# Optimization experiments

Measured on AMD Instinct MI355X. Metric: run time of the kernel, lower is better.

## Reference

```python
import jax, jax.numpy as jnp
import numpy as np

B, N, C, OUT, K2 = 64, 4096, 64, 64, 4  # batch, lattice sites, in/out features, kersize^2

def setup_inputs() -> dict:
    key = jax.random.key(0)
    k1, k2, k3, k4 = jax.random.split(key, 4)
    std = 0.5 / jnp.sqrt(K2 * (C + OUT))  # matches module's init stddev (W_scale=b_scale=1)
    x = jax.random.normal(k1, (B, N, C), dtype=jnp.float32)
    W = jax.random.normal(k2, (K2, C, OUT), dtype=jnp.float32) * std
    b = jax.random.normal(k3, (OUT,), dtype=jnp.float32) * std
    kernel2 = jax.random.randint(k4, (N, K2), 0, N, dtype=jnp.int32)
    return {"x": x, "W": W, "b": b, "kernel2": kernel2}

def reference(x, W, b, kernel2):
    # gather neighbors: [B, N, K2, C]; contract (K2, C) with W -> [B, N, OUT]
    y = jnp.einsum('bnkc,kco->bno', x[:, kernel2, :], W)
    # bias broadcast (original used tensordot with ones([B,N]))
    return y + b
```

## Files before the change

kernel.cpp:

```cpp
#include <hip/hip_runtime.h>
#include <stdint.h>


#define N_SITES  4096
#define C_DIM    64
#define OUT_DIM  64

typedef __attribute__((ext_vector_type(8))) short bf16x8;
typedef __attribute__((ext_vector_type(4))) float f32x4;

__device__ __forceinline__ uint32_t pack2_bf16(float f0, float f1) {
    uint32_t u0 = __float_as_uint(f0) + 0x8000u;
    uint32_t u1 = __float_as_uint(f1) + 0x8000u;
    return __builtin_amdgcn_perm(u1, u0, 0x07060302u);
}

template<int N> __device__ __forceinline__ void wait_vmcnt() {
    asm volatile("s_waitcnt vmcnt(%0)" :: "n"(N) : "memory");
}

template<int OFF>
__device__ __forceinline__ void gld16(f32x4& d, const float* p) {
    asm volatile("global_load_dwordx4 %0, %1, off offset:%2"
                 : "=v"(d) : "v"(p), "n"(OFF) : "memory");
}

__host__ __device__ constexpr int wait_for(int i) {
    return (i == 0 || i == 1) ? 16
         : (i == 2)           ? 20
         : (i == 14)          ? 16
         : (i == 15)          ? 4
         : (i & 1)            ? 20
         : 24;
}

__global__ __launch_bounds__(64, 1)
void conv_vgather_kernel(const float* __restrict__ x, const float* __restrict__ W,
                         const float* __restrict__ bias, const int* __restrict__ kernel2,
                         float* __restrict__ out)
{
    __shared__ __align__(16) int lds_idx[32 * 4];

    const int lane = threadIdx.x;
    const int bi   = blockIdx.x;
    const int half = bi >> 10;
    const int r    = bi & 1023;
    const int bgl  = r & 7;
    const int sg   = r >> 3;
    const int bg   = bgl + half * 8;
    const int n0   = sg * 32;
    const int b0   = bg * 4;

    const int c  = lane & 15;
    const int q  = lane >> 4;
    const int sl = c >> 2;
    const int bb = c & 3;

    if (lane < 32)
        ((int4*)lds_idx)[lane] = ((const int4*)kernel2)[n0 + lane];

    bf16x8 aw[4][8];
    #pragma unroll
    for (int t = 0; t < 4; ++t)
        #pragma unroll
        for (int s = 0; s < 8; ++s) {
            uint32_t* ap = (uint32_t*)&aw[t][s];
            #pragma unroll
            for (int u = 0; u < 4; ++u) {
                float f0 = W[(size_t)(s*32 + q*8 + 2*u    ) * OUT_DIM + t*16 + c];
                float f1 = W[(size_t)(s*32 + q*8 + 2*u + 1) * OUT_DIM + t*16 + c];
                ap[u] = pack2_bf16(f0, f1);
            }
        }

    f32x4 bias_r[4];
    #pragma unroll
    for (int t = 0; t < 4; ++t) bias_r[t] = *(const f32x4*)&bias[t*16 + q*4];

    const float* gxb = x + (size_t)(b0 + bb) * (N_SITES * C_DIM) + q * 8;

    wait_vmcnt<0>();
    __builtin_amdgcn_sched_barrier(0);

    f32x4 buf0[8], buf1[8], buf2[8];

    auto issue = [&](f32x4* buf, int i) {
        const int2 tk = *(const int2*)&lds_idx[(i >> 1) * 16 + sl * 4 + (i & 1) * 2];
        const float* p0 = gxb + (size_t)(uint32_t)tk.x * C_DIM;
        const float* p1 = gxb + (size_t)(uint32_t)tk.y * C_DIM;
        gld16<0>(buf[0], p0); gld16<16>(buf[1], p0);
        gld16<128>(buf[2], p0); gld16<144>(buf[3], p0);
        gld16<0>(buf[4], p1); gld16<16>(buf[5], p1);
        gld16<128>(buf[6], p1); gld16<144>(buf[7], p1);
    };

    auto comp = [&](const f32x4* buf, int h, f32x4* acc) {
        #pragma unroll
        for (int tl = 0; tl < 2; ++tl)
            #pragma unroll
            for (int hs = 0; hs < 2; ++hs) {
                const f32x4 xa = buf[tl*4 + hs*2];
                const f32x4 xb = buf[tl*4 + hs*2 + 1];
                bf16x8 bf;
                uint32_t* bp = (uint32_t*)&bf;
                bp[0] = pack2_bf16(xa[0], xa[1]);
                bp[1] = pack2_bf16(xa[2], xa[3]);
                bp[2] = pack2_bf16(xb[0], xb[1]);
                bp[3] = pack2_bf16(xb[2], xb[3]);
                #pragma unroll
                for (int t = 0; t < 4; ++t)
                    acc[t] = __builtin_amdgcn_mfma_f32_16x16x32_bf16(
                        aw[t][h*4 + tl*2 + hs], bf, acc[t], 0, 0, 0);
            }
    };

    auto dostore = [&](int p, const f32x4* acc) {
        const int n = n0 + p * 4 + sl;
        float* op = out + ((size_t)(b0 + bb) * N_SITES + n) * OUT_DIM + q * 4;
        #pragma unroll
        for (int t = 0; t < 4; ++t)
            *(f32x4*)(op + t*16) = acc[t] + bias_r[t];
    };

    issue(buf0, 0);
    issue(buf1, 1);
    issue(buf2, 2);

    f32x4 acc[4];

    #define STEP(i)                                                           \
    {                                                                         \
        wait_vmcnt<wait_for(i)>();                                            \
        __builtin_amdgcn_sched_barrier(0);                                    \
        f32x4* bcur = ((i) % 3 == 0) ? buf0 : ((i) % 3 == 1) ? buf1 : buf2;   \
        if (((i) & 1) == 0) {                                                 \
            acc[0] = (f32x4){0.f,0.f,0.f,0.f};                                \
            acc[1] = (f32x4){0.f,0.f,0.f,0.f};                                \
            acc[2] = (f32x4){0.f,0.f,0.f,0.f};                                \
            acc[3] = (f32x4){0.f,0.f,0.f,0.f};                                \
        }                                                                     \
        comp(bcur, (i) & 1, acc);                                             \
        if ((i) <= 12) issue(bcur, (i) + 3);                                  \
        if ((i) & 1) dostore((i) >> 1, acc);                                  \
    }

    STEP(0);  STEP(1);  STEP(2);  STEP(3);
    STEP(4);  STEP(5);  STEP(6);  STEP(7);
    STEP(8);  STEP(9);  STEP(10); STEP(11);
    STEP(12); STEP(13); STEP(14); STEP(15);

    #undef STEP
}

extern "C" void kernel_launch(void* const* d_in, const int* in_sizes, int n_in,
                              void* d_out, int out_size, void* d_ws, size_t ws_size,
                              hipStream_t stream) {
    const float* x       = (const float*)d_in[0];
    const float* W       = (const float*)d_in[1];
    const float* bias    = (const float*)d_in[2];
    const int*   kernel2 = (const int*)d_in[3];
    float* out = (float*)d_out;

    conv_vgather_kernel<<<2048, 64, 0, stream>>>(x, W, bias, kernel2, out);
}
```

Measured before the change: 146.0 us.

## Split neighbor gathers between direct-to-LDS loads and register loads

Each pipeline step now sends one of its two gathered neighbor rows through global_load_lds_dwordx4 into a triple-buffered, XOR-swizzled LDS tile. The other row still goes through ordinary global loads into registers. The compute stage reads the LDS half with ds_reads before converting to bf16 for the MFMAs. The aim is to cut VGPR buffer pressure and spread load traffic across two paths. The cost is extra LDS traffic, m0 setup per load, and reliance on vmcnt ordering to know when LDS writes are visible.

```diff
diff --git a/kernel.cpp b/kernel.cpp
--- a/kernel.cpp
+++ b/kernel.cpp
@@ -17,6 +17,12 @@
 
 template<int N> __device__ __forceinline__ void wait_vmcnt() {
     asm volatile("s_waitcnt vmcnt(%0)" :: "n"(N) : "memory");
+}
+
+__device__ __forceinline__ void gll16(const float* p, uint32_t m0v) {
+    asm volatile("s_mov_b32 m0, %1\n\t"
+                 "global_load_lds_dwordx4 %0, off"
+                 :: "v"(p), "s"(m0v) : "memory");
 }
 
 template<int OFF>
@@ -35,11 +41,11 @@
 }
 
 __global__ __launch_bounds__(64, 1)
-void conv_vgather_kernel(const float* __restrict__ x, const float* __restrict__ W,
-                         const float* __restrict__ bias, const int* __restrict__ kernel2,
-                         float* __restrict__ out)
+void conv_dual_kernel(const float* __restrict__ x, const float* __restrict__ W,
+                      const float* __restrict__ bias, const int* __restrict__ kernel2,
+                      float* __restrict__ out)
 {
-    __shared__ __align__(16) int lds_idx[32 * 4];
+    __shared__ __align__(1024) uint8_t lds_raw[12800];
 
     const int lane = threadIdx.x;
     const int bi   = blockIdx.x;
@@ -56,8 +62,12 @@
     const int sl = c >> 2;
     const int bb = c & 3;
 
+    const int g = lane >> 4;
+    const int u = lane & 15;
+
     if (lane < 32)
-        ((int4*)lds_idx)[lane] = ((const int4*)kernel2)[n0 + lane];
+        ((int4*)(lds_raw + 12288))[lane] = ((const int4*)kernel2)[n0 + lane];
+    const int* lds_idx = (const int*)(lds_raw + 12288);
 
     bf16x8 aw[4][8];
     #pragma unroll
@@ -66,10 +76,10 @@
         for (int s = 0; s < 8; ++s) {
             uint32_t* ap = (uint32_t*)&aw[t][s];
             #pragma unroll
-            for (int u = 0; u < 4; ++u) {
-                float f0 = W[(size_t)(s*32 + q*8 + 2*u    ) * OUT_DIM + t*16 + c];
-                float f1 = W[(size_t)(s*32 + q*8 + 2*u + 1) * OUT_DIM + t*16 + c];
-                ap[u] = pack2_bf16(f0, f1);
+            for (int uu = 0; uu < 4; ++uu) {
+                float f0 = W[(size_t)(s*32 + q*8 + 2*uu    ) * OUT_DIM + t*16 + c];
+                float f1 = W[(size_t)(s*32 + q*8 + 2*uu + 1) * OUT_DIM + t*16 + c];
+                ap[uu] = pack2_bf16(f0, f1);
             }
         }
 
@@ -77,41 +87,69 @@
     #pragma unroll
     for (int t = 0; t < 4; ++t) bias_r[t] = *(const f32x4*)&bias[t*16 + q*4];
 
+    const float* gxn = x + (size_t)(b0 + g) * (N_SITES * C_DIM)
+                     + (size_t)((((u >> 1) ^ g) * 8) + (u & 1) * 4);
     const float* gxb = x + (size_t)(b0 + bb) * (N_SITES * C_DIM) + q * 8;
+
+    const uint32_t lds0 =
+        __builtin_amdgcn_readfirstlane((uint32_t)(uintptr_t)lds_raw);
 
     wait_vmcnt<0>();
     __builtin_amdgcn_sched_barrier(0);
 
-    f32x4 buf0[8], buf1[8], buf2[8];
-
-    auto issue = [&](f32x4* buf, int i) {
-        const int2 tk = *(const int2*)&lds_idx[(i >> 1) * 16 + sl * 4 + (i & 1) * 2];
-        const float* p0 = gxb + (size_t)(uint32_t)tk.x * C_DIM;
-        const float* p1 = gxb + (size_t)(uint32_t)tk.y * C_DIM;
-        gld16<0>(buf[0], p0); gld16<16>(buf[1], p0);
-        gld16<128>(buf[2], p0); gld16<144>(buf[3], p0);
-        gld16<0>(buf[4], p1); gld16<16>(buf[5], p1);
-        gld16<128>(buf[6], p1); gld16<144>(buf[7], p1);
+    f32x4 vb0[4], vb1[4], vb2[4];
+
+    auto issue = [&](f32x4* vb, int i) {
+        const int pp = i >> 1, h = i & 1;
+        const int* ib = lds_idx + pp * 16;
+        const uint32_t m0s = lds0 + (uint32_t)(i % 3) * 4096;
+        #pragma unroll
+        for (int slp = 0; slp < 4; ++slp) {
+            const int nka = ib[slp * 4 + 2 * h];
+            const float* rowa = gxn + (size_t)(uint32_t)nka * C_DIM;
+            gll16(rowa, m0s + (uint32_t)slp * 1024);
+        }
+        const int nkb = ib[sl * 4 + 2 * h + 1];
+        const float* rowb = gxb + (size_t)(uint32_t)nkb * C_DIM;
+        gld16<0>(vb[0], rowb);   gld16<16>(vb[1], rowb);
+        gld16<128>(vb[2], rowb); gld16<144>(vb[3], rowb);
     };
 
-    auto comp = [&](const f32x4* buf, int h, f32x4* acc) {
-        #pragma unroll
-        for (int tl = 0; tl < 2; ++tl)
+    auto comp = [&](const f32x4* vb, int i, f32x4* acc) {
+        const uint32_t tb = (uint32_t)(i % 3) * 4096;
+        const int h = i & 1;
+        #pragma unroll
+        for (int hs = 0; hs < 2; ++hs) {
+            const uint8_t* pb = lds_raw + tb + (uint32_t)c * 256
+                              + (uint32_t)(((hs * 4 + q) ^ (c & 3)) * 32);
+            f32x4 xa = *(const f32x4*)(pb);
+            f32x4 xb = *(const f32x4*)(pb + 16);
+            bf16x8 bf;
+            uint32_t* bp = (uint32_t*)&bf;
+            bp[0] = pack2_bf16(xa[0], xa[1]);
+            bp[1] = pack2_bf16(xa[2], xa[3]);
+            bp[2] = pack2_bf16(xb[0], xb[1]);
+            bp[3] = pack2_bf16(xb[2], xb[3]);
             #pragma unroll
-            for (int hs = 0; hs < 2; ++hs) {
-                const f32x4 xa = buf[tl*4 + hs*2];
-                const f32x4 xb = buf[tl*4 + hs*2 + 1];
-                bf16x8 bf;
-                uint32_t* bp = (uint32_t*)&bf;
-                bp[0] = pack2_bf16(xa[0], xa[1]);
-                bp[1] = pack2_bf16(xa[2], xa[3]);
-                bp[2] = pack2_bf16(xb[0], xb[1]);
-                bp[3] = pack2_bf16(xb[2], xb[3]);
-                #pragma unroll
-                for (int t = 0; t < 4; ++t)
-                    acc[t] = __builtin_amdgcn_mfma_f32_16x16x32_bf16(
-                        aw[t][h*4 + tl*2 + hs], bf, acc[t], 0, 0, 0);
-            }
+            for (int t = 0; t < 4; ++t)
+                acc[t] = __builtin_amdgcn_mfma_f32_16x16x32_bf16(
+                    aw[t][h*4 + hs], bf, acc[t], 0, 0, 0);
+        }
+        #pragma unroll
+        for (int hs = 0; hs < 2; ++hs) {
+            const f32x4 xa = vb[hs*2];
+            const f32x4 xb = vb[hs*2 + 1];
+            bf16x8 bf;
+            uint32_t* bp = (uint32_t*)&bf;
+            bp[0] = pack2_bf16(xa[0], xa[1]);
+            bp[1] = pack2_bf16(xa[2], xa[3]);
+            bp[2] = pack2_bf16(xb[0], xb[1]);
+            bp[3] = pack2_bf16(xb[2], xb[3]);
+            #pragma unroll
+            for (int t = 0; t < 4; ++t)
+                acc[t] = __builtin_amdgcn_mfma_f32_16x16x32_bf16(
+                    aw[t][h*4 + 2 + hs], bf, acc[t], 0, 0, 0);
+        }
     };
 
     auto dostore = [&](int p, const f32x4* acc) {
@@ -122,9 +160,9 @@
             *(f32x4*)(op + t*16) = acc[t] + bias_r[t];
     };
 
-    issue(buf0, 0);
-    issue(buf1, 1);
-    issue(buf2, 2);
+    issue(vb0, 0);
+    issue(vb1, 1);
+    issue(vb2, 2);
 
     f32x4 acc[4];
 
@@ -132,14 +170,14 @@
     {                                                                         \
         wait_vmcnt<wait_for(i)>();                                            \
         __builtin_amdgcn_sched_barrier(0);                                    \
-        f32x4* bcur = ((i) % 3 == 0) ? buf0 : ((i) % 3 == 1) ? buf1 : buf2;   \
+        f32x4* bcur = ((i) % 3 == 0) ? vb0 : ((i) % 3 == 1) ? vb1 : vb2;      \
         if (((i) & 1) == 0) {                                                 \
             acc[0] = (f32x4){0.f,0.f,0.f,0.f};                                \
             acc[1] = (f32x4){0.f,0.f,0.f,0.f};                                \
             acc[2] = (f32x4){0.f,0.f,0.f,0.f};                                \
             acc[3] = (f32x4){0.f,0.f,0.f,0.f};                                \
         }                                                                     \
-        comp(bcur, (i) & 1, acc);                                             \
+        comp(bcur, (i), acc);                                                 \
         if ((i) <= 12) issue(bcur, (i) + 3);                                  \
         if ((i) & 1) dostore((i) >> 1, acc);                                  \
     }
@@ -161,5 +199,5 @@
     const int*   kernel2 = (const int*)d_in[3];
     float* out = (float*)d_out;
 
-    conv_vgather_kernel<<<2048, 64, 0, stream>>>(x, W, bias, kernel2, out);
-}
+    conv_dual_kernel<<<2048, 64, 0, stream>>>(x, W, bias, kernel2, out);
+}
```

New measurement: 140.2 us. 1.04x faster.
